# Performance work log

Measured on AMD Instinct MI355X. Metric: run time of the kernel, lower is better.

Reference implementation:

```python
import jax, jax.numpy as jnp
import numpy as np

EMBED_DIM = 1024
NUM_HEADS = 16
HEAD_DIM = EMBED_DIM // NUM_HEADS

def setup_inputs() -> dict:
    key = jax.random.key(0)
    k1, k2, k3 = jax.random.split(key, 3)
    x = jax.random.normal(k1, (4, 2048, EMBED_DIM), dtype=jnp.float32)
    # Linear weights stored as [out, in] like torch; we apply x @ W.T
    W_qkv = jax.random.normal(k2, (3 * EMBED_DIM, EMBED_DIM), dtype=jnp.float32) * (EMBED_DIM ** -0.5)
    W_proj = jax.random.normal(k3, (EMBED_DIM, EMBED_DIM), dtype=jnp.float32) * (EMBED_DIM ** -0.5)
    return {"x": x, "W_qkv": W_qkv, "W_proj": W_proj}

def reference(x, W_qkv, W_proj):
    B, T, C = x.shape
    H, D = NUM_HEADS, HEAD_DIM
    qkv = x @ W_qkv.T                          # [B,T,3C]
    q, k, v = jnp.split(qkv, 3, axis=-1)
    q = q.reshape(B, T, H, D).transpose(0, 2, 1, 3)  # [B,H,T,D]
    k = k.reshape(B, T, H, D).transpose(0, 2, 1, 3)
    v = v.reshape(B, T, H, D).transpose(0, 2, 1, 3)
    scores = jnp.einsum('bhqd,bhkd->bhqk', q, k) / jnp.sqrt(jnp.asarray(D, x.dtype))
    causal = jnp.tril(jnp.ones((T, T), dtype=bool))
    scores = jnp.where(causal, scores, -jnp.inf)
    weights = jax.nn.softmax(scores, axis=-1)
    out = jnp.einsum('bhqk,bhkd->bhqd', weights, v)  # [B,H,T,D]
    out = out.transpose(0, 2, 1, 3).reshape(B, T, C)
    return out @ W_proj.T
```

## Files before the change

### kernel.cpp

```cpp
#include <hip/hip_runtime.h>

#define T_SEQ 2048
#define NB 4
#define NH 16
#define HD 64
#define CDIM 1024
#define MROWS (NB * T_SEQ)

typedef __attribute__((ext_vector_type(8))) short short8;
typedef __attribute__((ext_vector_type(4))) float floatx4;

static __device__ __forceinline__ unsigned short f2bf(float f) {
  union { float f; unsigned int i; } c; c.f = f;
  return (unsigned short)((c.i + 0x7FFFu + ((c.i >> 16) & 1u)) >> 16);
}
static __device__ __forceinline__ unsigned short f2bf_trunc(float f) {
  union { float f; unsigned int i; } c; c.f = f;
  return (unsigned short)(c.i >> 16);
}

static __device__ __forceinline__ void gl2lds16(const void* g, void* l) {
  __builtin_amdgcn_global_load_lds(
      (const __attribute__((address_space(1))) unsigned int*)g,
      (__attribute__((address_space(3))) unsigned int*)l, 16, 0, 0);
}

__global__ __launch_bounds__(256) void cast_bf16(const float* __restrict__ in,
                                                 unsigned short* __restrict__ out,
                                                 const int n4) {
  const int i = blockIdx.x * 256 + threadIdx.x;
  if (i < n4) {
    const float4 v = ((const float4*)in)[i];
    ushort4 o;
    o.x = f2bf(v.x); o.y = f2bf(v.y); o.z = f2bf(v.z); o.w = f2bf(v.w);
    ((ushort4*)out)[i] = o;
  }
}

#define Q_PRESCALE 0.18033688f

__global__ __launch_bounds__(256) void gemm_bf16_qkv(
    const unsigned short* __restrict__ A,
    const unsigned short* __restrict__ B,
    unsigned short* __restrict__ Oq,
    unsigned short* __restrict__ Ok,
    unsigned short* __restrict__ Ovt,
    const int K)
{
  __shared__ unsigned short As[128 * 32];
  __shared__ unsigned short Bs[128 * 32];
  const int tid = threadIdx.x;
  const int w = tid >> 6, l = tid & 63;
  const int quad = l >> 4, l15 = l & 15;
  const int m0 = blockIdx.y * 128, n0 = blockIdx.x * 128;
  const int wm = (w >> 1) * 64, wn = (w & 1) * 64;
  const int srow = l >> 2, scol = (l & 3) * 8;

  floatx4 acc[4][4];
#pragma unroll
  for (int mi = 0; mi < 4; ++mi)
#pragma unroll
    for (int ni = 0; ni < 4; ++ni) acc[mi][ni] = (floatx4){0.f, 0.f, 0.f, 0.f};

  const unsigned short* Ag = A + (size_t)(m0 + w * 32 + srow) * K + scol;
  const unsigned short* Bg = B + (size_t)(n0 + w * 32 + srow) * K + scol;
  unsigned short* Al0 = &As[(w * 32) * 32];
  unsigned short* Al1 = &As[(w * 32 + 16) * 32];
  unsigned short* Bl0 = &Bs[(w * 32) * 32];
  unsigned short* Bl1 = &Bs[(w * 32 + 16) * 32];

  for (int k0 = 0; k0 < K; k0 += 32) {
    __syncthreads();
    gl2lds16(Ag + k0, Al0);
    gl2lds16(Ag + (size_t)16 * K + k0, Al1);
    gl2lds16(Bg + k0, Bl0);
    gl2lds16(Bg + (size_t)16 * K + k0, Bl1);
    __syncthreads();
    short8 af[4], bfr[4];
#pragma unroll
    for (int mi = 0; mi < 4; ++mi)
      af[mi] = *(const short8*)&As[(wm + mi * 16 + l15) * 32 + quad * 8];
#pragma unroll
    for (int ni = 0; ni < 4; ++ni)
      bfr[ni] = *(const short8*)&Bs[(wn + ni * 16 + l15) * 32 + quad * 8];
#pragma unroll
    for (int mi = 0; mi < 4; ++mi)
#pragma unroll
      for (int ni = 0; ni < 4; ++ni)
        acc[mi][ni] = __builtin_amdgcn_mfma_f32_16x16x32_bf16(af[mi], bfr[ni], acc[mi][ni], 0, 0, 0);
  }

  const int mbase = m0 + wm + quad * 4;
#pragma unroll
  for (int ni = 0; ni < 4; ++ni) {
    const int n = n0 + wn + ni * 16 + l15;
    const int which = n >> 10;
    const int h = (n >> 6) & (NH - 1), d = n & (HD - 1);
    if (which == 2) {
#pragma unroll
      for (int mi = 0; mi < 4; ++mi) {
        const int m = mbase + mi * 16;
        const int b = m >> 11, t0 = m & (T_SEQ - 1);
        ushort4 pk;
        pk.x = f2bf(acc[mi][ni][0]); pk.y = f2bf(acc[mi][ni][1]);
        pk.z = f2bf(acc[mi][ni][2]); pk.w = f2bf(acc[mi][ni][3]);
        *(ushort4*)(Ovt + ((size_t)((b * NH + h) * HD + d) << 11) + t0) = pk;
      }
    } else {
      unsigned short* dst = (which == 0) ? Oq : Ok;
      const float sc = (which == 0) ? Q_PRESCALE : 1.0f;
#pragma unroll
      for (int mi = 0; mi < 4; ++mi)
#pragma unroll
        for (int r = 0; r < 4; ++r) {
          const int m = mbase + mi * 16 + r;
          const int b = m >> 11, t = m & (T_SEQ - 1);
          dst[(((size_t)(b * NH + h) * T_SEQ + t) << 6) + d] = f2bf(acc[mi][ni][r] * sc);
        }
    }
  }
}

__global__ __launch_bounds__(256) void gemm_bf16_proj(
    const unsigned short* __restrict__ A,
    const unsigned short* __restrict__ B,
    float* __restrict__ O,
    const int N, const int K)
{
  __shared__ unsigned short As[128 * 32];
  __shared__ unsigned short Bs[128 * 32];
  const int tid = threadIdx.x;
  const int w = tid >> 6, l = tid & 63;
  const int quad = l >> 4, l15 = l & 15;
  const int m0 = blockIdx.y * 128, n0 = blockIdx.x * 128;
  const int wm = (w >> 1) * 64, wn = (w & 1) * 64;
  const int srow = l >> 2, scol = (l & 3) * 8;

  floatx4 acc[4][4];
#pragma unroll
  for (int mi = 0; mi < 4; ++mi)
#pragma unroll
    for (int ni = 0; ni < 4; ++ni) acc[mi][ni] = (floatx4){0.f, 0.f, 0.f, 0.f};

  const unsigned short* Ag = A + (size_t)(m0 + w * 32 + srow) * K + scol;
  const unsigned short* Bg = B + (size_t)(n0 + w * 32 + srow) * K + scol;
  unsigned short* Al0 = &As[(w * 32) * 32];
  unsigned short* Al1 = &As[(w * 32 + 16) * 32];
  unsigned short* Bl0 = &Bs[(w * 32) * 32];
  unsigned short* Bl1 = &Bs[(w * 32 + 16) * 32];

  for (int k0 = 0; k0 < K; k0 += 32) {
    __syncthreads();
    gl2lds16(Ag + k0, Al0);
    gl2lds16(Ag + (size_t)16 * K + k0, Al1);
    gl2lds16(Bg + k0, Bl0);
    gl2lds16(Bg + (size_t)16 * K + k0, Bl1);
    __syncthreads();
    short8 af[4], bfr[4];
#pragma unroll
    for (int mi = 0; mi < 4; ++mi)
      af[mi] = *(const short8*)&As[(wm + mi * 16 + l15) * 32 + quad * 8];
#pragma unroll
    for (int ni = 0; ni < 4; ++ni)
      bfr[ni] = *(const short8*)&Bs[(wn + ni * 16 + l15) * 32 + quad * 8];
#pragma unroll
    for (int mi = 0; mi < 4; ++mi)
#pragma unroll
      for (int ni = 0; ni < 4; ++ni)
        acc[mi][ni] = __builtin_amdgcn_mfma_f32_16x16x32_bf16(af[mi], bfr[ni], acc[mi][ni], 0, 0, 0);
  }

#pragma unroll
  for (int mi = 0; mi < 4; ++mi)
#pragma unroll
    for (int r = 0; r < 4; ++r) {
      const int m = m0 + wm + mi * 16 + quad * 4 + r;
#pragma unroll
      for (int ni = 0; ni < 4; ++ni)
        O[(size_t)m * N + n0 + wn + ni * 16 + l15] = acc[mi][ni][r];
    }
}

#define TK 64
#define KROW 72
#define PROW 68

__global__ __launch_bounds__(512) void attn_mfma(
    const unsigned short* __restrict__ Q,
    const unsigned short* __restrict__ K,
    const unsigned short* __restrict__ Vt,
    unsigned short* __restrict__ O)
{
  __shared__ unsigned short Ks[TK * KROW];
  __shared__ unsigned short Vts[HD * KROW];
  __shared__ unsigned short Pw[8][16 * PROW];
  const int tid = threadIdx.x;
  const int w = tid >> 6, l = tid & 63;
  const int quad = l >> 4, l15 = l & 15;
  const int prow = tid >> 3, pch = (tid & 7) * 8;

  const int bh = blockIdx.x & 63;
  const int pp = blockIdx.x >> 6;
  const int b = bh >> 4, h = bh & 15;
  const size_t hoff = (size_t)bh * T_SEQ * HD;
  const unsigned short* Qh = Q + hoff;
  const unsigned short* Kh = K + hoff;
  const unsigned short* Vth = Vt + hoff;

  short8 ones;
#pragma unroll
  for (int j = 0; j < 8; ++j) ones[j] = (short)0x3F80;

#pragma unroll 1
  for (int ii = 0; ii < 2; ++ii) {
    const int qtile = ii ? pp : (15 - pp);
    const int qw = qtile * 128 + w * 16;

    short8 qf[2];
    {
      const int qrow = qw + l15;
      qf[0] = *(const short8*)(Qh + (size_t)qrow * HD + quad * 8);
      qf[1] = *(const short8*)(Qh + (size_t)qrow * HD + 32 + quad * 8);
    }

    floatx4 Of[4];
#pragma unroll
    for (int dc = 0; dc < 4; ++dc) Of[dc] = (floatx4){0.f, 0.f, 0.f, 0.f};
    floatx4 lacc = (floatx4){0.f, 0.f, 0.f, 0.f};

    const int nkt = 2 * qtile + 2;
    uint4 kr = *(const uint4*)(Kh + (size_t)prow * HD + pch);
    uint4 vr = *(const uint4*)(Vth + ((size_t)prow << 11) + pch);

    for (int kt = 0; kt < nkt; ++kt) {
      const int kt0 = kt * TK;
      __syncthreads();
      *(uint4*)&Ks[prow * KROW + pch] = kr;
      *(uint4*)&Vts[prow * KROW + pch] = vr;
      __syncthreads();
      if (kt + 1 < nkt) {
        const int nt0 = kt0 + TK;
        kr = *(const uint4*)(Kh + (size_t)(nt0 + prow) * HD + pch);
        vr = *(const uint4*)(Vth + ((size_t)prow << 11) + nt0 + pch);
      }

      if (qw + 15 >= kt0) {
        floatx4 Sf[4];
#pragma unroll
        for (int cb = 0; cb < 4; ++cb) {
          Sf[cb] = (floatx4){0.f, 0.f, 0.f, 0.f};
#pragma unroll
          for (int h2 = 0; h2 < 2; ++h2) {
            const short8 kf = *(const short8*)&Ks[(cb * 16 + l15) * KROW + h2 * 32 + quad * 8];
            Sf[cb] = __builtin_amdgcn_mfma_f32_16x16x32_bf16(qf[h2], kf, Sf[cb], 0, 0, 0);
          }
        }
        const bool full = (kt0 + 63 <= qw);
        if (full) {
#pragma unroll
          for (int cb = 0; cb < 4; ++cb)
#pragma unroll
            for (int r = 0; r < 4; ++r)
              Pw[w][(quad * 4 + r) * PROW + cb * 16 + l15] = f2bf_trunc(exp2f(Sf[cb][r]));
        } else {
#pragma unroll
          for (int cb = 0; cb < 4; ++cb) {
            const int key = kt0 + cb * 16 + l15;
#pragma unroll
            for (int r = 0; r < 4; ++r) {
              const int qrow = qw + quad * 4 + r;
              const float p = (key > qrow) ? 0.f : exp2f(Sf[cb][r]);
              Pw[w][(quad * 4 + r) * PROW + cb * 16 + l15] = f2bf_trunc(p);
            }
          }
        }
#pragma unroll
        for (int kg = 0; kg < 2; ++kg) {
          const short8 pf = *(const short8*)&Pw[w][l15 * PROW + kg * 32 + quad * 8];
          lacc = __builtin_amdgcn_mfma_f32_16x16x32_bf16(pf, ones, lacc, 0, 0, 0);
#pragma unroll
          for (int dc = 0; dc < 4; ++dc) {
            const short8 vf = *(const short8*)&Vts[(dc * 16 + l15) * KROW + kg * 32 + quad * 8];
            Of[dc] = __builtin_amdgcn_mfma_f32_16x16x32_bf16(pf, vf, Of[dc], 0, 0, 0);
          }
        }
      }
    }

#pragma unroll
    for (int r = 0; r < 4; ++r) {
      const float inv = 1.f / lacc[r];
      const int q = qw + quad * 4 + r;
#pragma unroll
      for (int dc = 0; dc < 4; ++dc)
        O[(size_t)(b * T_SEQ + q) * CDIM + h * HD + dc * 16 + l15] = f2bf(Of[dc][r] * inv);
    }
  }
}

extern "C" void kernel_launch(void* const* d_in, const int* in_sizes, int n_in,
                              void* d_out, int out_size, void* d_ws, size_t ws_size,
                              hipStream_t stream) {
  const float* x     = (const float*)d_in[0];
  const float* Wqkv  = (const float*)d_in[1];
  const float* Wproj = (const float*)d_in[2];
  float* out = (float*)d_out;

  const size_t XSZ = (size_t)MROWS * CDIM;
  const size_t WQSZ = (size_t)3 * CDIM * CDIM;
  const size_t WPSZ = (size_t)CDIM * CDIM;
  unsigned short* xb  = (unsigned short*)d_ws;
  unsigned short* wqb = xb + XSZ;
  unsigned short* wpb = wqb + WQSZ;
  unsigned short* qbuf = wpb + WPSZ;
  unsigned short* kbuf = qbuf + XSZ;
  unsigned short* vtbuf = kbuf + XSZ;
  unsigned short* abuf = vtbuf + XSZ;

  cast_bf16<<<XSZ / 4 / 256, 256, 0, stream>>>(x, xb, (int)(XSZ / 4));
  cast_bf16<<<WQSZ / 4 / 256, 256, 0, stream>>>(Wqkv, wqb, (int)(WQSZ / 4));
  cast_bf16<<<WPSZ / 4 / 256, 256, 0, stream>>>(Wproj, wpb, (int)(WPSZ / 4));

  dim3 g1(3 * CDIM / 128, MROWS / 128);
  gemm_bf16_qkv<<<g1, 256, 0, stream>>>(xb, wqb, qbuf, kbuf, vtbuf, CDIM);

  attn_mfma<<<512, 512, 0, stream>>>(qbuf, kbuf, vtbuf, abuf);

  dim3 g3(CDIM / 128, MROWS / 128);
  gemm_bf16_proj<<<g3, 256, 0, stream>>>(abuf, wpb, out, CDIM, CDIM);
}
```

Measured before the change: 267.0 us.

## Swizzle LDS layouts, use direct global-to-LDS loads in attention, merge cast kernels

Merges the three fp32-to-bf16 cast launches into one kernel over the contiguous workspace, saving two launches. Both GEMMs get an XOR swizzle on the LDS column chunk to cut bank conflicts on the MFMA operand reads. The attention kernel switches its K/V tile staging from register prefetch plus padded-row LDS stores to global_load_lds DMA into an unpadded, XOR-swizzled layout. This frees registers and LDS but gives up the explicit register prefetch overlap, so each tile's load is now exposed between the barriers.

```diff
diff --git a/kernel.cpp b/kernel.cpp
--- a/kernel.cpp
+++ b/kernel.cpp
@@ -25,16 +25,22 @@
       (__attribute__((address_space(3))) unsigned int*)l, 16, 0, 0);
 }
 
-__global__ __launch_bounds__(256) void cast_bf16(const float* __restrict__ in,
-                                                 unsigned short* __restrict__ out,
-                                                 const int n4) {
+#define X4 (MROWS * CDIM / 4)
+#define WQ4 (3 * CDIM * CDIM / 4)
+#define WP4 (CDIM * CDIM / 4)
+__global__ __launch_bounds__(256) void cast3_bf16(const float* __restrict__ x,
+                                                  const float* __restrict__ wq,
+                                                  const float* __restrict__ wp,
+                                                  unsigned short* __restrict__ out) {
   const int i = blockIdx.x * 256 + threadIdx.x;
-  if (i < n4) {
-    const float4 v = ((const float4*)in)[i];
-    ushort4 o;
-    o.x = f2bf(v.x); o.y = f2bf(v.y); o.z = f2bf(v.z); o.w = f2bf(v.w);
-    ((ushort4*)out)[i] = o;
-  }
+  const float* src; int off;
+  if (i < X4) { src = x; off = i; }
+  else if (i < X4 + WQ4) { src = wq; off = i - X4; }
+  else { src = wp; off = i - X4 - WQ4; }
+  const float4 v = ((const float4*)src)[off];
+  ushort4 o;
+  o.x = f2bf(v.x); o.y = f2bf(v.y); o.z = f2bf(v.z); o.w = f2bf(v.w);
+  ((ushort4*)out)[i] = o;
 }
 
 #define Q_PRESCALE 0.18033688f
@@ -54,7 +60,8 @@
   const int quad = l >> 4, l15 = l & 15;
   const int m0 = blockIdx.y * 128, n0 = blockIdx.x * 128;
   const int wm = (w >> 1) * 64, wn = (w & 1) * 64;
-  const int srow = l >> 2, scol = (l & 3) * 8;
+  const int srow = l >> 2;
+  const int scol = ((l & 3) ^ (srow & 3)) * 8;
 
   floatx4 acc[4][4];
 #pragma unroll
@@ -68,6 +75,7 @@
   unsigned short* Al1 = &As[(w * 32 + 16) * 32];
   unsigned short* Bl0 = &Bs[(w * 32) * 32];
   unsigned short* Bl1 = &Bs[(w * 32 + 16) * 32];
+  const int sq = quad ^ (l15 & 3);
 
   for (int k0 = 0; k0 < K; k0 += 32) {
     __syncthreads();
@@ -79,10 +87,10 @@
     short8 af[4], bfr[4];
 #pragma unroll
     for (int mi = 0; mi < 4; ++mi)
-      af[mi] = *(const short8*)&As[(wm + mi * 16 + l15) * 32 + quad * 8];
+      af[mi] = *(const short8*)&As[(wm + mi * 16 + l15) * 32 + sq * 8];
 #pragma unroll
     for (int ni = 0; ni < 4; ++ni)
-      bfr[ni] = *(const short8*)&Bs[(wn + ni * 16 + l15) * 32 + quad * 8];
+      bfr[ni] = *(const short8*)&Bs[(wn + ni * 16 + l15) * 32 + sq * 8];
 #pragma unroll
     for (int mi = 0; mi < 4; ++mi)
 #pragma unroll
@@ -134,7 +142,8 @@
   const int quad = l >> 4, l15 = l & 15;
   const int m0 = blockIdx.y * 128, n0 = blockIdx.x * 128;
   const int wm = (w >> 1) * 64, wn = (w & 1) * 64;
-  const int srow = l >> 2, scol = (l & 3) * 8;
+  const int srow = l >> 2;
+  const int scol = ((l & 3) ^ (srow & 3)) * 8;
 
   floatx4 acc[4][4];
 #pragma unroll
@@ -148,6 +157,7 @@
   unsigned short* Al1 = &As[(w * 32 + 16) * 32];
   unsigned short* Bl0 = &Bs[(w * 32) * 32];
   unsigned short* Bl1 = &Bs[(w * 32 + 16) * 32];
+  const int sq = quad ^ (l15 & 3);
 
   for (int k0 = 0; k0 < K; k0 += 32) {
     __syncthreads();
@@ -159,10 +169,10 @@
     short8 af[4], bfr[4];
 #pragma unroll
     for (int mi = 0; mi < 4; ++mi)
-      af[mi] = *(const short8*)&As[(wm + mi * 16 + l15) * 32 + quad * 8];
+      af[mi] = *(const short8*)&As[(wm + mi * 16 + l15) * 32 + sq * 8];
 #pragma unroll
     for (int ni = 0; ni < 4; ++ni)
-      bfr[ni] = *(const short8*)&Bs[(wn + ni * 16 + l15) * 32 + quad * 8];
+      bfr[ni] = *(const short8*)&Bs[(wn + ni * 16 + l15) * 32 + sq * 8];
 #pragma unroll
     for (int mi = 0; mi < 4; ++mi)
 #pragma unroll
@@ -182,8 +192,6 @@
 }
 
 #define TK 64
-#define KROW 72
-#define PROW 68
 
 __global__ __launch_bounds__(512) void attn_mfma(
     const unsigned short* __restrict__ Q,
@@ -191,21 +199,25 @@
     const unsigned short* __restrict__ Vt,
     unsigned short* __restrict__ O)
 {
-  __shared__ unsigned short Ks[TK * KROW];
-  __shared__ unsigned short Vts[HD * KROW];
-  __shared__ unsigned short Pw[8][16 * PROW];
+  __shared__ unsigned short Ks[TK * HD];
+  __shared__ unsigned short Vts[HD * TK];
+  __shared__ unsigned short Pw[8][16 * 68];
   const int tid = threadIdx.x;
   const int w = tid >> 6, l = tid & 63;
   const int quad = l >> 4, l15 = l & 15;
-  const int prow = tid >> 3, pch = (tid & 7) * 8;
+  const int drow = 8 * w + (l >> 3);
+  const int dch = ((l & 7) ^ (l >> 3)) * 8;
+  const int sw7 = l15 & 7;
 
   const int bh = blockIdx.x & 63;
   const int pp = blockIdx.x >> 6;
   const int b = bh >> 4, h = bh & 15;
   const size_t hoff = (size_t)bh * T_SEQ * HD;
   const unsigned short* Qh = Q + hoff;
-  const unsigned short* Kh = K + hoff;
-  const unsigned short* Vth = Vt + hoff;
+  const unsigned short* Kdma = K + hoff + (size_t)drow * HD + dch;
+  const unsigned short* Vdma = Vt + hoff + ((size_t)drow << 11) + dch;
+  unsigned short* KsW = &Ks[w * 512];
+  unsigned short* VtsW = &Vts[w * 512];
 
   short8 ones;
 #pragma unroll
@@ -229,29 +241,23 @@
     floatx4 lacc = (floatx4){0.f, 0.f, 0.f, 0.f};
 
     const int nkt = 2 * qtile + 2;
-    uint4 kr = *(const uint4*)(Kh + (size_t)prow * HD + pch);
-    uint4 vr = *(const uint4*)(Vth + ((size_t)prow << 11) + pch);
-
     for (int kt = 0; kt < nkt; ++kt) {
       const int kt0 = kt * TK;
       __syncthreads();
-      *(uint4*)&Ks[prow * KROW + pch] = kr;
-      *(uint4*)&Vts[prow * KROW + pch] = vr;
+      gl2lds16(Kdma + (size_t)kt0 * HD, KsW);
+      gl2lds16(Vdma + kt0, VtsW);
       __syncthreads();
-      if (kt + 1 < nkt) {
-        const int nt0 = kt0 + TK;
-        kr = *(const uint4*)(Kh + (size_t)(nt0 + prow) * HD + pch);
-        vr = *(const uint4*)(Vth + ((size_t)prow << 11) + nt0 + pch);
-      }
 
       if (qw + 15 >= kt0) {
         floatx4 Sf[4];
 #pragma unroll
         for (int cb = 0; cb < 4; ++cb) {
           Sf[cb] = (floatx4){0.f, 0.f, 0.f, 0.f};
+          const int krow = cb * 16 + l15;
 #pragma unroll
           for (int h2 = 0; h2 < 2; ++h2) {
-            const short8 kf = *(const short8*)&Ks[(cb * 16 + l15) * KROW + h2 * 32 + quad * 8];
+            const int ch = (h2 * 4 + quad) ^ sw7;
+            const short8 kf = *(const short8*)&Ks[krow * 64 + ch * 8];
             Sf[cb] = __builtin_amdgcn_mfma_f32_16x16x32_bf16(qf[h2], kf, Sf[cb], 0, 0, 0);
           }
         }
@@ -261,7 +267,7 @@
           for (int cb = 0; cb < 4; ++cb)
 #pragma unroll
             for (int r = 0; r < 4; ++r)
-              Pw[w][(quad * 4 + r) * PROW + cb * 16 + l15] = f2bf_trunc(exp2f(Sf[cb][r]));
+              Pw[w][(quad * 4 + r) * 68 + cb * 16 + l15] = f2bf_trunc(exp2f(Sf[cb][r]));
         } else {
 #pragma unroll
           for (int cb = 0; cb < 4; ++cb) {
@@ -270,17 +276,19 @@
             for (int r = 0; r < 4; ++r) {
               const int qrow = qw + quad * 4 + r;
               const float p = (key > qrow) ? 0.f : exp2f(Sf[cb][r]);
-              Pw[w][(quad * 4 + r) * PROW + cb * 16 + l15] = f2bf_trunc(p);
+              Pw[w][(quad * 4 + r) * 68 + cb * 16 + l15] = f2bf_trunc(p);
             }
           }
         }
 #pragma unroll
         for (int kg = 0; kg < 2; ++kg) {
-          const short8 pf = *(const short8*)&Pw[w][l15 * PROW + kg * 32 + quad * 8];
+          const short8 pf = *(const short8*)&Pw[w][l15 * 68 + kg * 32 + quad * 8];
           lacc = __builtin_amdgcn_mfma_f32_16x16x32_bf16(pf, ones, lacc, 0, 0, 0);
 #pragma unroll
           for (int dc = 0; dc < 4; ++dc) {
-            const short8 vf = *(const short8*)&Vts[(dc * 16 + l15) * KROW + kg * 32 + quad * 8];
+            const int vrow = dc * 16 + l15;
+            const int ch = (kg * 4 + quad) ^ sw7;
+            const short8 vf = *(const short8*)&Vts[vrow * 64 + ch * 8];
             Of[dc] = __builtin_amdgcn_mfma_f32_16x16x32_bf16(pf, vf, Of[dc], 0, 0, 0);
           }
         }
@@ -317,9 +325,7 @@
   unsigned short* vtbuf = kbuf + XSZ;
   unsigned short* abuf = vtbuf + XSZ;
 
-  cast_bf16<<<XSZ / 4 / 256, 256, 0, stream>>>(x, xb, (int)(XSZ / 4));
-  cast_bf16<<<WQSZ / 4 / 256, 256, 0, stream>>>(Wqkv, wqb, (int)(WQSZ / 4));
-  cast_bf16<<<WPSZ / 4 / 256, 256, 0, stream>>>(Wproj, wpb, (int)(WPSZ / 4));
+  cast3_bf16<<<(X4 + WQ4 + WP4) / 256, 256, 0, stream>>>(x, Wqkv, Wproj, xb);
 
   dim3 g1(3 * CDIM / 128, MROWS / 128);
   gemm_bf16_qkv<<<g1, 256, 0, stream>>>(xb, wqb, qbuf, kbuf, vtbuf, CDIM);
```

After: 266.7 us. No clear change (-0.1%).
